# Kernel optimization log

Hardware: AMD Instinct MI355X
Metric: run time of the kernel (lower is better)

## Reference

```python
import jax, jax.numpy as jnp
import numpy as np

# ASPPConv constants (from init_kwargs)
K = 9                      # kernel_size
DILATION = 6
PAD = DILATION * (K // 2)  # 24, 'same' padding for dilated conv
SIGMA = DILATION * 1.0     # self.sigma = dilation * sigma
BN_EPS = 1e-5


def setup_inputs() -> dict:
    key = jax.random.key(0)
    k1, k2, k3 = jax.random.split(key, 3)
    B, C, O, L = 8, 256, 16384, 0  # placeholder to keep names readable
    B, Cin, Cout, L = 8, 256, 256, 16384
    x = jax.random.normal(k1, (B, Cin, L), dtype=jnp.float32)
    coords = jax.random.uniform(k2, (B, 3, L), dtype=jnp.float32)  # xyz per point
    weight = jax.random.normal(k3, (Cout, Cin, K), dtype=jnp.float32) * 0.05
    gamma = jnp.ones((Cout,), jnp.float32)
    beta = jnp.zeros((Cout,), jnp.float32)
    return {"x": x, "coords": coords, "weight": weight, "gamma": gamma, "beta": beta}


def _weighted_conv1d(x, coords, weight):
    """Dilated conv1d where each tap is scaled by a Gaussian of the squared
    euclidean distance between the tap's coordinates and the center point's
    coordinates: w_k = exp(-||c_k - c_center||^2 / (2*sigma^2)).
    Zero padding (matches F.unfold) for both x and coords."""
    B, C, L = x.shape
    x_pad = jnp.pad(x, ((0, 0), (0, 0), (PAD, PAD)))
    c_pad = jnp.pad(coords, ((0, 0), (0, 0), (PAD, PAD)))
    inv_2s2 = 1.0 / (2.0 * SIGMA * SIGMA)
    out = jnp.zeros((B, weight.shape[0], L), x.dtype)
    # K=9 taps: small fixed loop; avoids materializing the [B,C,K,L] unfold.
    for k in range(K):
        off = k * DILATION
        xk = jax.lax.dynamic_slice_in_dim(x_pad, off, L, axis=2)   # [B,C,L]
        ck = jax.lax.dynamic_slice_in_dim(c_pad, off, L, axis=2)   # [B,3,L]
        dist2 = jnp.sum((ck - coords) ** 2, axis=1)                # [B,L]
        wk = jnp.exp(-dist2 * inv_2s2)                             # [B,L]
        out = out + jnp.einsum('bcl,oc->bol', xk * wk[:, None, :], weight[:, :, k])
    return out


def reference(x, coords, weight, gamma, beta):
    y = _weighted_conv1d(x, coords, weight)                        # [B,O,L]
    # BatchNorm1d (training mode): stats over batch and length per channel
    mean = jnp.mean(y, axis=(0, 2), keepdims=True)
    var = jnp.var(y, axis=(0, 2), keepdims=True)
    y = (y - mean) * jax.lax.rsqrt(var + BN_EPS)
    y = y * gamma[None, :, None] + beta[None, :, None]
    return jax.nn.relu(y)
```

## Files before the change

kernel.cpp:

```cpp
#include <hip/hip_runtime.h>
#include <hip/hip_bf16.h>

#define LEN   16384
#define CIN   256
#define COUT  256
#define NB    8
#define NTAP  9
#define DIL   6
#define PADW  24
#define NSTEP 72

typedef __bf16 bf16x8 __attribute__((ext_vector_type(8)));
typedef float  f32x4  __attribute__((ext_vector_type(4)));
typedef unsigned short u16;
typedef u16 u16x8 __attribute__((ext_vector_type(8)));

#define WKT_BYTES  (NB*NTAP*LEN*4)
#define WB_BYTES   (NSTEP*256*32*2)
#define SUMS_OFF   (WKT_BYTES + WB_BYTES)
#define SCB_OFF    (SUMS_OFF + 512*4)

__global__ __launch_bounds__(256) void k_wk(const float* __restrict__ coords,
                                            float* __restrict__ wkt) {
    int i = blockIdx.x * 256 + threadIdx.x;
    if (i >= NB * NTAP * LEN) return;
    int l = i & (LEN - 1);
    int bk = i >> 14;
    int k = bk % NTAP, b = bk / NTAP;
    const float* cb = coords + (size_t)b * 3 * LEN;
    int lt = l + k * DIL - PADW;
    bool ok = (unsigned)lt < (unsigned)LEN;
    float d2 = 0.f;
#pragma unroll
    for (int j = 0; j < 3; ++j) {
        float cc = cb[j * LEN + l];
        float ct = ok ? cb[j * LEN + lt] : 0.f;
        float d = ct - cc;
        d2 += d * d;
    }
    wkt[i] = expf(-d2 * (1.f / 72.f));
}

__global__ __launch_bounds__(256) void k_wb(const float* __restrict__ W,
                                            u16* __restrict__ Wb) {
    int i = blockIdx.x * 256 + threadIdx.x;
    if (i >= NSTEP * 256 * 32) return;
    int j = i & 31;
    int o = (i >> 5) & 255;
    int s = i >> 13;
    int k = s >> 3;
    int c = ((s & 7) << 5) + j;
    float v = W[((size_t)o * CIN + c) * NTAP + k];
    unsigned u = __builtin_bit_cast(unsigned, v);
    u += 0x7FFFu + ((u >> 16) & 1u);
    Wb[i] = (u16)(u >> 16);
}

__global__ __launch_bounds__(256, 2) void k_conv(
    const float* __restrict__ x,
    const float* __restrict__ wkt,
    const u16*   __restrict__ Wb,
    float* __restrict__ y,
    float* __restrict__ sums)
{
    const int lt = blockIdx.x;
    const int ob = blockIdx.y;
    const int b  = blockIdx.z;
    const int l0 = lt * 128;
    const int tid  = threadIdx.x;
    const int lane = tid & 63;
    const int wid  = tid >> 6;
    const int wr = wid >> 1;
    const int wc = wid & 1;

    __shared__ u16 As[2][128 * 40];
    __shared__ u16 Bs[2][128 * 40];

    f32x4 acc[4][4] = {};

    const int sl  = tid & 127;
    const int cg0 = tid >> 7;

    bf16x8 aReg[2];
    float  xReg[16];
    float  wkv;

    auto stage_load = [&](int s) {
        const int ktap  = s >> 3;
        const int cbase = (s & 7) << 5;
        const u16* wsrc = Wb + ((size_t)s * 256 + ob * 128) * 32;
#pragma unroll
        for (int i = 0; i < 2; ++i) {
            int idx = i * 256 + tid;
            int o = idx >> 2, kc = idx & 3;
            aReg[i] = *reinterpret_cast<const bf16x8*>(wsrc + o * 32 + kc * 8);
        }
        const int gx = l0 + sl + ktap * DIL - PADW;
        const bool ok = (unsigned)gx < (unsigned)LEN;
        const float* xb = x + (size_t)b * CIN * LEN + gx;
#pragma unroll
        for (int g = 0; g < 2; ++g) {
            int c = cbase + (cg0 + g * 2) * 8;
#pragma unroll
            for (int j = 0; j < 8; ++j)
                xReg[g * 8 + j] = ok ? xb[(size_t)(c + j) * LEN] : 0.f;
        }
        wkv = wkt[((size_t)b * NTAP + ktap) * LEN + l0 + sl];
    };

    auto stage_write = [&](int bufi) {
#pragma unroll
        for (int i = 0; i < 2; ++i) {
            int idx = i * 256 + tid;
            int o = idx >> 2, kc = idx & 3;
            *reinterpret_cast<bf16x8*>(&As[bufi][o * 40 + kc * 8]) = aReg[i];
        }
#pragma unroll
        for (int g = 0; g < 2; ++g) {
            int cg = cg0 + g * 2;
            u16x8 bv;
#pragma unroll
            for (int j = 0; j < 8; ++j) {
                float v = xReg[g * 8 + j] * wkv;
                unsigned u = __builtin_bit_cast(unsigned, v);
                u += 0x7FFFu + ((u >> 16) & 1u);
                bv[j] = (u16)(u >> 16);
            }
            *reinterpret_cast<u16x8*>(&Bs[bufi][sl * 40 + cg * 8]) = bv;
        }
    };

    stage_load(0);
    stage_write(0);
    __syncthreads();

    const int fr  = lane & 15;
    const int kc4 = (lane >> 4) * 8;

    for (int s = 0; s < NSTEP; ++s) {
        const int cur = s & 1;
        if (s < NSTEP - 1) stage_load(s + 1);
        bf16x8 af[4], bfv[4];
        const u16* Ab = &As[cur][(wr * 64 + fr) * 40 + kc4];
        const u16* Bb = &Bs[cur][(wc * 64 + fr) * 40 + kc4];
#pragma unroll
        for (int mi = 0; mi < 4; ++mi)
            af[mi] = *reinterpret_cast<const bf16x8*>(Ab + mi * 16 * 40);
#pragma unroll
        for (int ni = 0; ni < 4; ++ni)
            bfv[ni] = *reinterpret_cast<const bf16x8*>(Bb + ni * 16 * 40);
#pragma unroll
        for (int mi = 0; mi < 4; ++mi)
#pragma unroll
            for (int ni = 0; ni < 4; ++ni)
                acc[mi][ni] = __builtin_amdgcn_mfma_f32_16x16x32_bf16(
                    af[mi], bfv[ni], acc[mi][ni], 0, 0, 0);
        if (s < NSTEP - 1) stage_write(cur ^ 1);
        __syncthreads();
    }

    const int col = lane & 15;
    const int rg  = lane >> 4;
    float* yb = y + ((size_t)b * COUT + ob * 128 + wr * 64) * LEN + l0 + wc * 64;
#pragma unroll
    for (int mi = 0; mi < 4; ++mi) {
#pragma unroll
        for (int r = 0; r < 4; ++r) {
            const int o_loc = mi * 16 + rg * 4 + r;
            float s1 = 0.f, s2 = 0.f;
#pragma unroll
            for (int ni = 0; ni < 4; ++ni) {
                float v = acc[mi][ni][r];
                yb[(size_t)o_loc * LEN + ni * 16 + col] = v;
                s1 += v;
                s2 += v * v;
            }
#pragma unroll
            for (int m = 1; m < 16; m <<= 1) {
                s1 += __shfl_xor(s1, m, 64);
                s2 += __shfl_xor(s2, m, 64);
            }
            if (col == 0) {
                int o = ob * 128 + wr * 64 + o_loc;
                atomicAdd(&sums[o], s1);
                atomicAdd(&sums[COUT + o], s2);
            }
        }
    }
}

__global__ __launch_bounds__(256) void k_stats(const float* __restrict__ sums,
                                               const float* __restrict__ gamma,
                                               const float* __restrict__ beta,
                                               float* __restrict__ scb) {
    int o = threadIdx.x;
    const float inv_n = 1.f / (float)(NB * LEN);
    float mean = sums[o] * inv_n;
    float var  = sums[COUT + o] * inv_n - mean * mean;
    float sc = gamma[o] * rsqrtf(var + 1e-5f);
    scb[o]        = sc;
    scb[COUT + o] = beta[o] - mean * sc;
}

__global__ __launch_bounds__(256) void k_norm(float* __restrict__ y,
                                              const float* __restrict__ scb) {
    const int total4 = NB * COUT * LEN / 4;
    int i = blockIdx.x * 256 + threadIdx.x;
    for (; i < total4; i += gridDim.x * 256) {
        f32x4 v = reinterpret_cast<f32x4*>(y)[i];
        int o = (i >> 12) & 255;
        float sc = scb[o], bi = scb[COUT + o];
#pragma unroll
        for (int j = 0; j < 4; ++j)
            v[j] = fmaxf(v[j] * sc + bi, 0.f);
        reinterpret_cast<f32x4*>(y)[i] = v;
    }
}

extern "C" void kernel_launch(void* const* d_in, const int* in_sizes, int n_in,
                              void* d_out, int out_size, void* d_ws, size_t ws_size,
                              hipStream_t stream) {
    const float* x      = (const float*)d_in[0];
    const float* coords = (const float*)d_in[1];
    const float* W      = (const float*)d_in[2];
    const float* gamma  = (const float*)d_in[3];
    const float* beta   = (const float*)d_in[4];
    float* out = (float*)d_out;
    char*  ws  = (char*)d_ws;

    float* wkt  = (float*)ws;
    u16*   Wb   = (u16*)(ws + WKT_BYTES);
    float* sums = (float*)(ws + SUMS_OFF);
    float* scb  = (float*)(ws + SCB_OFF);

    hipMemsetAsync(sums, 0, 512 * 4, stream);

    k_wk<<<(NB * NTAP * LEN + 255) / 256, 256, 0, stream>>>(coords, wkt);
    k_wb<<<(NSTEP * 256 * 32 + 255) / 256, 256, 0, stream>>>(W, Wb);

    dim3 g(LEN / 128, 2, NB);
    k_conv<<<g, 256, 0, stream>>>(x, wkt, Wb, out, sums);

    k_stats<<<1, 256, 0, stream>>>(sums, gamma, beta, scb);
    k_norm<<<2048, 256, 0, stream>>>(out, scb);
}
```

Baseline: 438.1 us.

## Pre-transpose x to padded bf16 and apply tap weights post-GEMM per tap

Adds a pre-pass that transposes x into a zero-padded, channel-contiguous bf16 layout. The conv kernel can then stream both operands straight into LDS with global_load_lds instead of doing strided fp32 gathers and converting in registers. The Gaussian tap weight is pulled out of the GEMM operand: each tap's partial accumulator is scaled by a per-column weight held in LDS and added into a final accumulator. This removes per-element multiply and conversion from the inner loop, but doubles accumulator registers, adds an extra pass over x, and drops the LDS padding, which may cause bank conflicts.

After: 454.6 us. 3.8% more time.

```diff
diff --git a/kernel.cpp b/kernel.cpp
--- a/kernel.cpp
+++ b/kernel.cpp
@@ -9,6 +9,7 @@
 #define DIL   6
 #define PADW  24
 #define NSTEP 72
+#define PADROWS (LEN + 2*PADW)
 
 typedef __bf16 bf16x8 __attribute__((ext_vector_type(8)));
 typedef float  f32x4  __attribute__((ext_vector_type(4)));
@@ -17,8 +18,20 @@
 
 #define WKT_BYTES  (NB*NTAP*LEN*4)
 #define WB_BYTES   (NSTEP*256*32*2)
-#define SUMS_OFF   (WKT_BYTES + WB_BYTES)
+#define XT_OFF     (WKT_BYTES + WB_BYTES)
+#define XT_BYTES   ((size_t)NB*PADROWS*256*2)
+#define SUMS_OFF   (XT_OFF + XT_BYTES)
 #define SCB_OFF    (SUMS_OFF + 512*4)
+
+#define GLOAD_LDS(g, l) __builtin_amdgcn_global_load_lds( \
+    (const __attribute__((address_space(1))) void*)(g),   \
+    (__attribute__((address_space(3))) void*)(l), 16, 0, 0)
+
+__device__ __forceinline__ u16 f2bf(float v) {
+    unsigned u = __builtin_bit_cast(unsigned, v);
+    u += 0x7FFFu + ((u >> 16) & 1u);
+    return (u16)(u >> 16);
+}
 
 __global__ __launch_bounds__(256) void k_wk(const float* __restrict__ coords,
                                             float* __restrict__ wkt) {
@@ -50,14 +63,47 @@
     int s = i >> 13;
     int k = s >> 3;
     int c = ((s & 7) << 5) + j;
-    float v = W[((size_t)o * CIN + c) * NTAP + k];
-    unsigned u = __builtin_bit_cast(unsigned, v);
-    u += 0x7FFFu + ((u >> 16) & 1u);
-    Wb[i] = (u16)(u >> 16);
+    Wb[i] = f2bf(W[((size_t)o * CIN + c) * NTAP + k]);
+}
+
+__global__ __launch_bounds__(256) void k_xt(const float* __restrict__ x,
+                                            u16* __restrict__ xt) {
+    __shared__ float t[64 * 65];
+    const int tid = threadIdx.x;
+    const int cg  = blockIdx.x;
+    const int rg  = blockIdx.y;
+    const int b   = blockIdx.z;
+    const int lx0 = rg * 64 - PADW;
+#pragma unroll
+    for (int i = 0; i < 4; ++i) {
+        int c  = i * 16 + (tid >> 4);
+        int l4 = (tid & 15) * 4;
+        int lx = lx0 + l4;
+        f32x4 v = {};
+        if (lx >= 0 && lx + 3 < LEN)
+            v = *reinterpret_cast<const f32x4*>(
+                x + ((size_t)b * CIN + cg * 64 + c) * LEN + lx);
+        float* tr = &t[c * 65 + l4];
+        tr[0] = v[0]; tr[1] = v[1]; tr[2] = v[2]; tr[3] = v[3];
+    }
+    __syncthreads();
+#pragma unroll
+    for (int m = 0; m < 2; ++m) {
+        int l    = m * 32 + (tid >> 3);
+        int c0   = (tid & 7) * 8;
+        int prow = rg * 64 + l;
+        if (prow < PADROWS) {
+            u16x8 o;
+#pragma unroll
+            for (int j = 0; j < 8; ++j) o[j] = f2bf(t[(c0 + j) * 65 + l]);
+            *reinterpret_cast<u16x8*>(
+                xt + ((size_t)b * PADROWS + prow) * 256 + cg * 64 + c0) = o;
+        }
+    }
 }
 
 __global__ __launch_bounds__(256, 2) void k_conv(
-    const float* __restrict__ x,
+    const u16*   __restrict__ xt,
     const float* __restrict__ wkt,
     const u16*   __restrict__ Wb,
     float* __restrict__ y,
@@ -73,94 +119,81 @@
     const int wr = wid >> 1;
     const int wc = wid & 1;
 
-    __shared__ u16 As[2][128 * 40];
-    __shared__ u16 Bs[2][128 * 40];
-
-    f32x4 acc[4][4] = {};
-
-    const int sl  = tid & 127;
-    const int cg0 = tid >> 7;
-
-    bf16x8 aReg[2];
-    float  xReg[16];
-    float  wkv;
-
-    auto stage_load = [&](int s) {
+    __shared__ u16 As[2][4096];
+    __shared__ u16 Bs[2][4096];
+    __shared__ float wkl[NTAP * 128];
+
+    for (int i = tid; i < NTAP * 128; i += 256) {
+        int k = i >> 7, l = i & 127;
+        wkl[i] = wkt[((size_t)b * NTAP + k) * LEN + l0 + l];
+    }
+
+    f32x4 acc_f[4][4] = {};
+    f32x4 acc_t[4][4] = {};
+
+    const u16* wbBase = Wb + (size_t)ob * 4096;
+    const u16* xtBase = xt + (size_t)b * PADROWS * 256;
+
+    auto stage = [&](int bufi, int s) {
         const int ktap  = s >> 3;
         const int cbase = (s & 7) << 5;
-        const u16* wsrc = Wb + ((size_t)s * 256 + ob * 128) * 32;
-#pragma unroll
-        for (int i = 0; i < 2; ++i) {
-            int idx = i * 256 + tid;
-            int o = idx >> 2, kc = idx & 3;
-            aReg[i] = *reinterpret_cast<const bf16x8*>(wsrc + o * 32 + kc * 8);
-        }
-        const int gx = l0 + sl + ktap * DIL - PADW;
-        const bool ok = (unsigned)gx < (unsigned)LEN;
-        const float* xb = x + (size_t)b * CIN * LEN + gx;
-#pragma unroll
-        for (int g = 0; g < 2; ++g) {
-            int c = cbase + (cg0 + g * 2) * 8;
-#pragma unroll
-            for (int j = 0; j < 8; ++j)
-                xReg[g * 8 + j] = ok ? xb[(size_t)(c + j) * LEN] : 0.f;
-        }
-        wkv = wkt[((size_t)b * NTAP + ktap) * LEN + l0 + sl];
+#pragma unroll
+        for (int j = 0; j < 2; ++j) {
+            const int q = wid * 2 + j;
+            const u16* ga = wbBase + (size_t)s * 8192 + q * 512 + lane * 8;
+            GLOAD_LDS(ga, &As[bufi][q * 512]);
+            const u16* gb = xtBase
+                + (size_t)(l0 + q * 16 + (lane >> 2) + 6 * ktap) * 256
+                + cbase + (lane & 3) * 8;
+            GLOAD_LDS(gb, &Bs[bufi][q * 512]);
+        }
     };
 
-    auto stage_write = [&](int bufi) {
-#pragma unroll
-        for (int i = 0; i < 2; ++i) {
-            int idx = i * 256 + tid;
-            int o = idx >> 2, kc = idx & 3;
-            *reinterpret_cast<bf16x8*>(&As[bufi][o * 40 + kc * 8]) = aReg[i];
-        }
-#pragma unroll
-        for (int g = 0; g < 2; ++g) {
-            int cg = cg0 + g * 2;
-            u16x8 bv;
-#pragma unroll
-            for (int j = 0; j < 8; ++j) {
-                float v = xReg[g * 8 + j] * wkv;
-                unsigned u = __builtin_bit_cast(unsigned, v);
-                u += 0x7FFFu + ((u >> 16) & 1u);
-                bv[j] = (u16)(u >> 16);
-            }
-            *reinterpret_cast<u16x8*>(&Bs[bufi][sl * 40 + cg * 8]) = bv;
-        }
-    };
-
-    stage_load(0);
-    stage_write(0);
+    stage(0, 0);
     __syncthreads();
 
     const int fr  = lane & 15;
     const int kc4 = (lane >> 4) * 8;
+    const int col = lane & 15;
+    const int rg  = lane >> 4;
 
     for (int s = 0; s < NSTEP; ++s) {
         const int cur = s & 1;
-        if (s < NSTEP - 1) stage_load(s + 1);
+        if (s < NSTEP - 1) stage(cur ^ 1, s + 1);
         bf16x8 af[4], bfv[4];
-        const u16* Ab = &As[cur][(wr * 64 + fr) * 40 + kc4];
-        const u16* Bb = &Bs[cur][(wc * 64 + fr) * 40 + kc4];
+        const u16* Ab = &As[cur][(wr * 64 + fr) * 32 + kc4];
+        const u16* Bb = &Bs[cur][(wc * 64 + fr) * 32 + kc4];
 #pragma unroll
         for (int mi = 0; mi < 4; ++mi)
-            af[mi] = *reinterpret_cast<const bf16x8*>(Ab + mi * 16 * 40);
+            af[mi] = *reinterpret_cast<const bf16x8*>(Ab + mi * 512);
 #pragma unroll
         for (int ni = 0; ni < 4; ++ni)
-            bfv[ni] = *reinterpret_cast<const bf16x8*>(Bb + ni * 16 * 40);
+            bfv[ni] = *reinterpret_cast<const bf16x8*>(Bb + ni * 512);
 #pragma unroll
         for (int mi = 0; mi < 4; ++mi)
 #pragma unroll
             for (int ni = 0; ni < 4; ++ni)
-                acc[mi][ni] = __builtin_amdgcn_mfma_f32_16x16x32_bf16(
-                    af[mi], bfv[ni], acc[mi][ni], 0, 0, 0);
-        if (s < NSTEP - 1) stage_write(cur ^ 1);
+                acc_t[mi][ni] = __builtin_amdgcn_mfma_f32_16x16x32_bf16(
+                    af[mi], bfv[ni], acc_t[mi][ni], 0, 0, 0);
+        if ((s & 7) == 7) {
+            const int ktap = s >> 3;
+            float wv[4];
+#pragma unroll
+            for (int ni = 0; ni < 4; ++ni)
+                wv[ni] = wkl[ktap * 128 + wc * 64 + ni * 16 + col];
+#pragma unroll
+            for (int mi = 0; mi < 4; ++mi)
+#pragma unroll
+                for (int ni = 0; ni < 4; ++ni) {
+#pragma unroll
+                    for (int r = 0; r < 4; ++r)
+                        acc_f[mi][ni][r] += wv[ni] * acc_t[mi][ni][r];
+                    acc_t[mi][ni] = f32x4{};
+                }
+        }
         __syncthreads();
     }
 
-    const int col = lane & 15;
-    const int rg  = lane >> 4;
     float* yb = y + ((size_t)b * COUT + ob * 128 + wr * 64) * LEN + l0 + wc * 64;
 #pragma unroll
     for (int mi = 0; mi < 4; ++mi) {
@@ -170,7 +203,7 @@
             float s1 = 0.f, s2 = 0.f;
 #pragma unroll
             for (int ni = 0; ni < 4; ++ni) {
-                float v = acc[mi][ni][r];
+                float v = acc_f[mi][ni][r];
                 yb[(size_t)o_loc * LEN + ni * 16 + col] = v;
                 s1 += v;
                 s2 += v * v;
@@ -230,6 +263,7 @@
 
     float* wkt  = (float*)ws;
     u16*   Wb   = (u16*)(ws + WKT_BYTES);
+    u16*   xtp  = (u16*)(ws + XT_OFF);
     float* sums = (float*)(ws + SUMS_OFF);
     float* scb  = (float*)(ws + SCB_OFF);
 
@@ -237,9 +271,10 @@
 
     k_wk<<<(NB * NTAP * LEN + 255) / 256, 256, 0, stream>>>(coords, wkt);
     k_wb<<<(NSTEP * 256 * 32 + 255) / 256, 256, 0, stream>>>(W, Wb);
+    k_xt<<<dim3(4, (PADROWS + 63) / 64, NB), 256, 0, stream>>>(x, xtp);
 
     dim3 g(LEN / 128, 2, NB);
-    k_conv<<<g, 256, 0, stream>>>(x, wkt, Wb, out, sums);
+    k_conv<<<g, 256, 0, stream>>>(xtp, wkt, Wb, out, sums);
 
     k_stats<<<1, 256, 0, stream>>>(sums, gamma, beta, scb);
     k_norm<<<2048, 256, 0, stream>>>(out, scb);
```
